# Kernel optimization log

Hardware: AMD Instinct MI355X
Metric: run time of the kernel (lower is better)

## Reference

```python
import jax, jax.numpy as jnp
import numpy as np

B, T, C, H, E, K = 4, 2048, 512, 2048, 8, 2


def setup_inputs() -> dict:
    key = jax.random.key(0)
    ks = jax.random.split(key, 7)
    s_r = 1.0 / np.sqrt(C)
    s_h = 1.0 / np.sqrt(H)
    return {
        "x": jax.random.normal(ks[0], (B, T, C), dtype=jnp.float32),
        "Wr": jax.random.uniform(ks[1], (C, E), jnp.float32, -s_r, s_r),
        "br": jax.random.uniform(ks[2], (E,), jnp.float32, -s_r, s_r),
        "W1": jax.random.uniform(ks[3], (E, C, H), jnp.float32, -s_r, s_r),
        "b1": jax.random.uniform(ks[4], (E, H), jnp.float32, -s_r, s_r),
        "W2": jax.random.uniform(ks[5], (E, H, C), jnp.float32, -s_h, s_h),
        "b2": jax.random.uniform(ks[6], (E, C), jnp.float32, -s_h, s_h),
    }


def reference(x, Wr, br, W1, b1, W2, b2):
    # Router logits [B,T,E]
    logits = jnp.einsum("btc,ce->bte", x, Wr) + br
    topk_vals, topk_idx = jax.lax.top_k(logits, K)  # [B,T,K]
    scores = jax.nn.softmax(topk_vals, axis=-1)  # softmax over the K selected
    # Combine weights per expert: gate[b,t,e] = sum_k scores[b,t,k]*(idx==e)
    onehot = jax.nn.one_hot(topk_idx, E, dtype=x.dtype)  # [B,T,K,E]
    gate = jnp.einsum("btk,btke->bte", scores, onehot)  # [B,T,E]
    # Dense-masked expert MLPs (tokens not routed to e have gate==0)
    h = jax.nn.relu(jnp.einsum("btc,ech->bteh", x, W1) + b1)  # [B,T,E,H]
    y = jnp.einsum("bteh,ehc->btec", h, W2) + b2  # [B,T,E,C]
    out = jnp.einsum("btec,bte->btc", y, gate)  # weighted combine
    return logits, topk_idx, out
```

## Files before the change

kernel.cpp:

```cpp
#include <hip/hip_runtime.h>
#include <hip/hip_bf16.h>

#define NTOK 8192
#define NASN 16384
#define C_ 512
#define H_ 2048
#define E_ 8
#define NCH 128
#define CHTOK 64
#define MAXT 136

typedef __bf16 bf16x8 __attribute__((ext_vector_type(8)));
typedef float f32x4 __attribute__((ext_vector_type(4)));

#define WS_COUNTS 0
#define WS_BASE   4096
#define WS_OFFS   8192
#define WS_T1S    8448
#define WS_INFO   8704
#define WS_TOKL   (WS_INFO + NTOK*16)
#define WS_SLOTS  (WS_TOKL + NASN*4)
#define WS_XBF    (WS_SLOTS + NTOK*8)
#define WS_W1B    (WS_XBF + (size_t)NTOK*C_*2)
#define WS_W2B    (WS_W1B + (size_t)E_*H_*C_*2)
#define WS_HS     (WS_W2B + (size_t)E_*H_*C_*2)
#define WS_YS     WS_XBF

__device__ __forceinline__ unsigned int f2bf(float f) {
  __hip_bfloat16 h = __float2bfloat16(f);
  return (unsigned int)*(unsigned short*)&h;
}
__device__ __forceinline__ float bf2f(unsigned int u) {
  return __int_as_float((u & 0xffffu) << 16);
}

__device__ __forceinline__ void g2l16(const unsigned short* g, unsigned short* l) {
  __builtin_amdgcn_global_load_lds(
      (const __attribute__((address_space(1))) unsigned int*)g,
      (__attribute__((address_space(3))) unsigned int*)l, 16, 0, 0);
}

__global__ __launch_bounds__(256) void k_router(
    const float* __restrict__ x, const float* __restrict__ Wr,
    const float* __restrict__ br, float* __restrict__ out_logits,
    float* __restrict__ out_idx, int4* __restrict__ info,
    int* __restrict__ counts, unsigned short* __restrict__ Xbf)
{
  int t = blockIdx.x * 4 + (threadIdx.x >> 6);
  int lane = threadIdx.x & 63;
  const float4* xr = (const float4*)(x + (size_t)t * C_);
  float4 x0 = xr[lane*2], x1 = xr[lane*2+1];
  uint4 pk;
  pk.x = f2bf(x0.x) | (f2bf(x0.y) << 16);
  pk.y = f2bf(x0.z) | (f2bf(x0.w) << 16);
  pk.z = f2bf(x1.x) | (f2bf(x1.y) << 16);
  pk.w = f2bf(x1.z) | (f2bf(x1.w) << 16);
  *(uint4*)(Xbf + (size_t)t * C_ + lane*8) = pk;

  float xs[8] = {x0.x,x0.y,x0.z,x0.w,x1.x,x1.y,x1.z,x1.w};
  float acc[8] = {0,0,0,0,0,0,0,0};
  #pragma unroll
  for (int j = 0; j < 8; j++) {
    const float4* w = (const float4*)(Wr + (size_t)(lane*8+j) * E_);
    float4 w0 = w[0], w1 = w[1];
    float we[8] = {w0.x,w0.y,w0.z,w0.w,w1.x,w1.y,w1.z,w1.w};
    #pragma unroll
    for (int e = 0; e < 8; e++) acc[e] += xs[j] * we[e];
  }
  #pragma unroll
  for (int off = 1; off < 64; off <<= 1) {
    #pragma unroll
    for (int e = 0; e < 8; e++) acc[e] += __shfl_xor(acc[e], off, 64);
  }
  #pragma unroll
  for (int e = 0; e < 8; e++) acc[e] += br[e];
  if (lane == 0) {
    #pragma unroll
    for (int e = 0; e < 8; e++) out_logits[t*8 + e] = acc[e];
    int i0 = 0; float v0 = acc[0];
    #pragma unroll
    for (int e = 1; e < 8; e++) if (acc[e] > v0) { v0 = acc[e]; i0 = e; }
    int i1 = -1; float v1 = -1e30f;
    #pragma unroll
    for (int e = 0; e < 8; e++) if (e != i0 && acc[e] > v1) { v1 = acc[e]; i1 = e; }
    float d = expf(v1 - v0);
    float s1 = d / (1.0f + d);
    float s0 = 1.0f - s1;
    out_idx[t*2]     = (float)i0;
    out_idx[t*2 + 1] = (float)i1;
    info[t] = make_int4(i0, i1, __float_as_int(s0), __float_as_int(s1));
    int ch = t >> 6;
    atomicAdd(&counts[ch*8 + i0], 1);
    atomicAdd(&counts[ch*8 + i1], 1);
  }
}

__global__ __launch_bounds__(256) void k_prefix(
    const int* __restrict__ counts, int* __restrict__ base,
    int* __restrict__ offs, int* __restrict__ t1s)
{
  __shared__ int lc[NCH*8];
  __shared__ int tot[8];
  __shared__ int off_s[9];
  int tid = threadIdx.x;
  for (int i = tid; i < NCH*8; i += 256) lc[i] = counts[i];
  __syncthreads();
  if (tid < 8) {
    int run = 0;
    for (int c = 0; c < NCH; c++) { int v = lc[c*8+tid]; lc[c*8+tid] = run; run += v; }
    tot[tid] = run;
  }
  __syncthreads();
  if (tid == 0) {
    int o = 0, t = 0;
    off_s[0] = 0; offs[0] = 0; t1s[0] = 0;
    for (int e = 0; e < 8; e++) {
      o += tot[e];
      off_s[e+1] = o; offs[e+1] = o;
      t += (tot[e] + 127) >> 7;
      t1s[e+1] = t;
    }
  }
  __syncthreads();
  for (int i = tid; i < NCH*8; i += 256) base[i] = off_s[i & 7] + lc[i];
}

__global__ __launch_bounds__(64) void k_scatter(
    const int4* __restrict__ info, const int* __restrict__ base,
    int* __restrict__ tokl, int2* __restrict__ slots2)
{
  __shared__ int cur[8];
  int c = blockIdx.x, tid = threadIdx.x;
  if (tid < 8) cur[tid] = base[c*8 + tid];
  __syncthreads();
  int t = c * CHTOK + tid;
  int4 nfo = info[t];
  int r0 = atomicAdd(&cur[nfo.x], 1);
  int r1 = atomicAdd(&cur[nfo.y], 1);
  tokl[r0] = t;
  tokl[r1] = t;
  slots2[t] = make_int2(r0, r1);
}

__global__ __launch_bounds__(256) void k_transpose(
    const float* __restrict__ in, unsigned short* __restrict__ outp, int R, int S)
{
  __shared__ float tile[32][33];
  size_t zo = (size_t)blockIdx.z * R * S;
  in += zo; outp += zo;
  int s0 = blockIdx.x * 32, r0 = blockIdx.y * 32;
  int tx = threadIdx.x, ty = threadIdx.y;
  #pragma unroll
  for (int i = 0; i < 4; i++)
    tile[ty + i*8][tx] = in[(size_t)(r0 + ty + i*8) * S + s0 + tx];
  __syncthreads();
  #pragma unroll
  for (int i = 0; i < 4; i++)
    outp[(size_t)(s0 + ty + i*8) * R + r0 + tx] = f2bf(tile[tx][ty + i*8]);
}

__global__ __launch_bounds__(256) void k_gemm1(
    const unsigned short* __restrict__ Xbf, const int* __restrict__ tokl,
    const unsigned short* __restrict__ W1b,
    const float* __restrict__ b1, unsigned short* __restrict__ Hs,
    const int* __restrict__ offs, const int* __restrict__ t1s)
{
  __shared__ __align__(16) unsigned short AB[2*128*64];
  unsigned short* Al = AB;
  unsigned short* Bl = AB + 128*64;
  int b = blockIdx.x;
  int mo = b >> 7, rr = b & 127;
  int n0 = (rr >> 3) * 128;
  int mt = mo*8 + (rr & 7);
  if (mt >= t1s[8]) return;
  int e = 0;
  #pragma unroll
  for (int i = 0; i < 7; i++) if (mt >= t1s[e+1]) e++;
  int row0 = offs[e] + (mt - t1s[e]) * 128;
  int rowEnd = offs[e+1];
  int tid = threadIdx.x, lane = tid & 63, w = tid >> 6;
  int wm = (w & 1) * 64, wn = (w >> 1) * 64;
  int quad = lane >> 4, l16 = lane & 15;
  const f32x4 zero = {0.f, 0.f, 0.f, 0.f};
  f32x4 acc[4][4];
  #pragma unroll
  for (int i = 0; i < 4; i++)
    #pragma unroll
    for (int j = 0; j < 4; j++) acc[i][j] = zero;
  const unsigned short* Bsrc = W1b + ((size_t)e * H_ + n0) * C_;

  const unsigned short* ga[4]; const unsigned short* gb[4];
  unsigned short* la[4]; unsigned short* lb[4];
  #pragma unroll
  for (int j = 0; j < 4; j++) {
    int L = (w*4 + j)*64 + lane;
    int row = L >> 3;
    int cc = (L & 7) ^ (row & 7);
    int gr = row0 + row; gr = gr < NASN-1 ? gr : NASN-1;
    int trow = tokl[gr];
    ga[j] = Xbf + (size_t)trow * C_ + cc*8;
    gb[j] = Bsrc + (size_t)row * C_ + cc*8;
    la[j] = Al + (w*4 + j)*512;
    lb[j] = Bl + (w*4 + j)*512;
  }
  int r7 = l16 & 7;

  for (int kk = 0; kk < C_; kk += 64) {
    #pragma unroll
    for (int j = 0; j < 4; j++) {
      g2l16(ga[j] + kk, la[j]);
      g2l16(gb[j] + kk, lb[j]);
    }
    __syncthreads();
    #pragma unroll
    for (int ks4 = 0; ks4 < 8; ks4 += 4) {
      int chunk = (ks4 + quad) ^ r7;
      bf16x8 af[4], bfr[4];
      #pragma unroll
      for (int i = 0; i < 4; i++)
        af[i] = *(const bf16x8*)&Al[(wm + i*16 + l16)*64 + chunk*8];
      #pragma unroll
      for (int j = 0; j < 4; j++)
        bfr[j] = *(const bf16x8*)&Bl[(wn + j*16 + l16)*64 + chunk*8];
      #pragma unroll
      for (int i = 0; i < 4; i++)
        #pragma unroll
        for (int j = 0; j < 4; j++)
          acc[i][j] = __builtin_amdgcn_mfma_f32_16x16x32_bf16(af[i], bfr[j], acc[i][j], 0, 0, 0);
    }
    __syncthreads();
  }

  unsigned short* Lt = AB + w*4096;
  #pragma unroll
  for (int j = 0; j < 4; j++) {
    int n = n0 + wn + j*16 + l16;
    float bias = b1[e * H_ + n];
    #pragma unroll
    for (int i = 0; i < 4; i++)
      #pragma unroll
      for (int r = 0; r < 4; r++) {
        float v = acc[i][j][r] + bias;
        Lt[(i*16 + quad*4 + r)*64 + j*16 + l16] = (unsigned short)f2bf(v > 0.f ? v : 0.f);
      }
  }
  #pragma unroll
  for (int it = 0; it < 8; it++) {
    int rloc = it*8 + (lane >> 3);
    int m = row0 + wm + rloc;
    uint4 vv = *(uint4*)&Lt[rloc*64 + (lane & 7)*8];
    if (m < rowEnd)
      *(uint4*)(Hs + (size_t)m * H_ + n0 + wn + (lane & 7)*8) = vv;
  }
}

__global__ __launch_bounds__(512) void k_gemm2(
    const unsigned short* __restrict__ Hs, const unsigned short* __restrict__ W2b,
    const float* __restrict__ b2, unsigned short* __restrict__ Ys,
    const int* __restrict__ offs, const int* __restrict__ t1s)
{
  __shared__ __align__(16) unsigned short AB[2*2*128*64];
  int b = blockIdx.x;
  int g = b >> 5, rr = b & 31;
  int n0 = (rr >> 3) * 128;
  int mt = g*8 + (rr & 7);
  if (mt >= t1s[8]) return;
  int e = 0;
  #pragma unroll
  for (int i = 0; i < 7; i++) if (mt >= t1s[e+1]) e++;
  int row0 = offs[e] + (mt - t1s[e]) * 128;
  int rowEnd = offs[e+1];
  int tid = threadIdx.x, lane = tid & 63, w = tid >> 6;
  int wq = w >> 1, kh = w & 1;
  int wm = (wq & 1) * 64, wn = (wq >> 1) * 64;
  int quad = lane >> 4, l16 = lane & 15;
  const f32x4 zero = {0.f, 0.f, 0.f, 0.f};
  f32x4 acc[4][4];
  #pragma unroll
  for (int i = 0; i < 4; i++)
    #pragma unroll
    for (int j = 0; j < 4; j++) acc[i][j] = zero;
  const unsigned short* Bsrc = W2b + ((size_t)e * C_ + n0) * H_;

  const unsigned short* ga[4]; const unsigned short* gb[4];
  unsigned short* la[4]; unsigned short* lb[4];
  #pragma unroll
  for (int j = 0; j < 4; j++) {
    int L = (wq*4 + j)*64 + lane;
    int row = L >> 3;
    int cc = (L & 7) ^ (row & 7);
    int gr = row0 + row; gr = gr < NASN-1 ? gr : NASN-1;
    ga[j] = Hs + (size_t)gr * H_ + kh*1024 + cc*8;
    gb[j] = Bsrc + (size_t)row * H_ + kh*1024 + cc*8;
    la[j] = AB + kh*16384 + (wq*4 + j)*512;
    lb[j] = AB + kh*16384 + 8192 + (wq*4 + j)*512;
  }
  int r7 = l16 & 7;
  const unsigned short* Ap = AB + kh*16384;
  const unsigned short* Bp = AB + kh*16384 + 8192;

  for (int kk = 0; kk < 1024; kk += 64) {
    #pragma unroll
    for (int j = 0; j < 4; j++) {
      g2l16(ga[j] + kk, la[j]);
      g2l16(gb[j] + kk, lb[j]);
    }
    __syncthreads();
    #pragma unroll
    for (int ks4 = 0; ks4 < 8; ks4 += 4) {
      int chunk = (ks4 + quad) ^ r7;
      bf16x8 af[4], bfr[4];
      #pragma unroll
      for (int i = 0; i < 4; i++)
        af[i] = *(const bf16x8*)&Ap[(wm + i*16 + l16)*64 + chunk*8];
      #pragma unroll
      for (int j = 0; j < 4; j++)
        bfr[j] = *(const bf16x8*)&Bp[(wn + j*16 + l16)*64 + chunk*8];
      #pragma unroll
      for (int i = 0; i < 4; i++)
        #pragma unroll
        for (int j = 0; j < 4; j++)
          acc[i][j] = __builtin_amdgcn_mfma_f32_16x16x32_bf16(af[i], bfr[j], acc[i][j], 0, 0, 0);
    }
    __syncthreads();
  }

  float* X = (float*)AB;
  if (kh == 1) {
    #pragma unroll
    for (int i = 0; i < 4; i++)
      #pragma unroll
      for (int j = 0; j < 4; j++) {
        int c = j*16 + l16;
        int slot = (i*4 + quad) ^ (c & 15);
        *(f32x4*)&X[wq*4096 + c*64 + slot*4] = acc[i][j];
      }
  }
  __syncthreads();
  if (kh == 0) {
    #pragma unroll
    for (int j = 0; j < 4; j++) {
      int c = j*16 + l16;
      float bias = b2[e * C_ + n0 + wn + c];
      #pragma unroll
      for (int i = 0; i < 4; i++) {
        int slot = (i*4 + quad) ^ (c & 15);
        f32x4 p = *(const f32x4*)&X[wq*4096 + c*64 + slot*4];
        #pragma unroll
        for (int r = 0; r < 4; r++) acc[i][j][r] += p[r] + bias;
      }
    }
  }
  __syncthreads();
  if (kh == 0) {
    unsigned short* Lt = AB + wq*4096;
    #pragma unroll
    for (int j = 0; j < 4; j++)
      #pragma unroll
      for (int i = 0; i < 4; i++)
        #pragma unroll
        for (int r = 0; r < 4; r++)
          Lt[(i*16 + quad*4 + r)*64 + j*16 + l16] =
              (unsigned short)f2bf(acc[i][j][r]);
    #pragma unroll
    for (int it = 0; it < 8; it++) {
      int rloc = it*8 + (lane >> 3);
      int m = row0 + wm + rloc;
      uint4 vv = *(uint4*)&Lt[rloc*64 + (lane & 7)*8];
      if (m < rowEnd)
        *(uint4*)(Ys + (size_t)m * C_ + n0 + wn + (lane & 7)*8) = vv;
    }
  }
}

__global__ __launch_bounds__(256) void k_combine(
    const unsigned short* __restrict__ Ys, const int4* __restrict__ info,
    const int2* __restrict__ slots2, float* __restrict__ outp)
{
  int t = blockIdx.x * 4 + (threadIdx.x >> 6);
  int lane = threadIdx.x & 63;
  int4 nfo = info[t];
  int2 ss = slots2[t];
  float g0 = __int_as_float(nfo.z), g1 = __int_as_float(nfo.w);
  uint4 a = *(const uint4*)(Ys + (size_t)ss.x * C_ + lane*8);
  uint4 bb = *(const uint4*)(Ys + (size_t)ss.y * C_ + lane*8);
  unsigned int au[4] = {a.x, a.y, a.z, a.w};
  unsigned int bu[4] = {bb.x, bb.y, bb.z, bb.w};
  float4 o0, o1;
  float* op = &o0.x;
  #pragma unroll
  for (int q = 0; q < 4; q++) {
    op[q*2 - (q>=2?0:0)] = 0;
  }
  float vals[8];
  #pragma unroll
  for (int q = 0; q < 4; q++) {
    vals[q*2]   = g0*bf2f(au[q])        + g1*bf2f(bu[q]);
    vals[q*2+1] = g0*bf2f(au[q] >> 16)  + g1*bf2f(bu[q] >> 16);
  }
  o0.x = vals[0]; o0.y = vals[1]; o0.z = vals[2]; o0.w = vals[3];
  o1.x = vals[4]; o1.y = vals[5]; o1.z = vals[6]; o1.w = vals[7];
  float4* o = (float4*)(outp + (size_t)t * C_ + lane*8);
  o[0] = o0;
  o[1] = o1;
}

extern "C" void kernel_launch(void* const* d_in, const int* in_sizes, int n_in,
                              void* d_out, int out_size, void* d_ws, size_t ws_size,
                              hipStream_t stream)
{
  const float* x  = (const float*)d_in[0];
  const float* Wr = (const float*)d_in[1];
  const float* br = (const float*)d_in[2];
  const float* W1 = (const float*)d_in[3];
  const float* b1 = (const float*)d_in[4];
  const float* W2 = (const float*)d_in[5];
  const float* b2 = (const float*)d_in[6];
  float* out = (float*)d_out;
  char* ws = (char*)d_ws;

  int*  counts = (int*)(ws + WS_COUNTS);
  int*  base   = (int*)(ws + WS_BASE);
  int*  offs   = (int*)(ws + WS_OFFS);
  int*  t1s    = (int*)(ws + WS_T1S);
  int4* info   = (int4*)(ws + WS_INFO);
  int*  tokl   = (int*)(ws + WS_TOKL);
  int2* slots2 = (int2*)(ws + WS_SLOTS);
  unsigned short* Xbf = (unsigned short*)(ws + WS_XBF);
  unsigned short* W1b = (unsigned short*)(ws + WS_W1B);
  unsigned short* W2b = (unsigned short*)(ws + WS_W2B);
  unsigned short* Hs  = (unsigned short*)(ws + WS_HS);
  unsigned short* Ys  = (unsigned short*)(ws + WS_YS);

  hipMemsetAsync(counts, 0, NCH*8*sizeof(int), stream);

  k_transpose<<<dim3(H_/32, C_/32, E_), dim3(32, 8), 0, stream>>>(W1, W1b, C_, H_);
  k_transpose<<<dim3(C_/32, H_/32, E_), dim3(32, 8), 0, stream>>>(W2, W2b, H_, C_);
  k_router<<<NTOK/4, 256, 0, stream>>>(x, Wr, br, out, out + 65536, info, counts, Xbf);
  k_prefix<<<1, 256, 0, stream>>>(counts, base, offs, t1s);
  k_scatter<<<NCH, 64, 0, stream>>>(info, base, tokl, slots2);
  k_gemm1<<<17*128, 256, 0, stream>>>(Xbf, tokl, W1b, b1, Hs, offs, t1s);
  k_gemm2<<<17*32, 512, 0, stream>>>(Hs, W2b, b2, Ys, offs, t1s);
  k_combine<<<NTOK/4, 256, 0, stream>>>(Ys, info, slots2, out + 81920);
}
```

Before: 305.7 us.

## Double-buffer GEMM K-loops and widen transpose tiles with vectorized bf16 stores

Both expert GEMMs now use a 32-wide K slice with two LDS buffers. The next slice's global-to-LDS copies are issued before computing the current one, and explicit vmcnt waits and barriers replace the two __syncthreads per step, so loads overlap with MFMA work. gemm2 drops its split-K across 512 threads and the cross-wave reduction through LDS, running 256 threads over the full H per block. That reduces waves per block and may lower latency hiding. The weight transpose now handles 128x32 tiles per block and writes four bf16 values per store.

```diff
diff --git a/kernel.cpp b/kernel.cpp
--- a/kernel.cpp
+++ b/kernel.cpp
@@ -8,7 +8,6 @@
 #define E_ 8
 #define NCH 128
 #define CHTOK 64
-#define MAXT 136
 
 typedef __bf16 bf16x8 __attribute__((ext_vector_type(8)));
 typedef float f32x4 __attribute__((ext_vector_type(4)));
@@ -145,18 +144,29 @@
 __global__ __launch_bounds__(256) void k_transpose(
     const float* __restrict__ in, unsigned short* __restrict__ outp, int R, int S)
 {
-  __shared__ float tile[32][33];
+  __shared__ float tile[128][33];
   size_t zo = (size_t)blockIdx.z * R * S;
   in += zo; outp += zo;
-  int s0 = blockIdx.x * 32, r0 = blockIdx.y * 32;
-  int tx = threadIdx.x, ty = threadIdx.y;
-  #pragma unroll
-  for (int i = 0; i < 4; i++)
-    tile[ty + i*8][tx] = in[(size_t)(r0 + ty + i*8) * S + s0 + tx];
+  int r0 = blockIdx.y * 128, s0 = blockIdx.x * 32;
+  int t = threadIdx.x;
+  #pragma unroll
+  for (int i = 0; i < 16; i++) {
+    int lin = i*256 + t;
+    int rr = lin >> 5, ss = lin & 31;
+    tile[rr][ss] = in[(size_t)(r0 + rr) * S + s0 + ss];
+  }
   __syncthreads();
   #pragma unroll
-  for (int i = 0; i < 4; i++)
-    outp[(size_t)(s0 + ty + i*8) * R + r0 + tx] = f2bf(tile[tx][ty + i*8]);
+  for (int i = 0; i < 4; i++) {
+    int lin = i*256 + t;
+    int ss = lin >> 5, rq = lin & 31;
+    ushort4 v;
+    v.x = (unsigned short)f2bf(tile[rq*4+0][ss]);
+    v.y = (unsigned short)f2bf(tile[rq*4+1][ss]);
+    v.z = (unsigned short)f2bf(tile[rq*4+2][ss]);
+    v.w = (unsigned short)f2bf(tile[rq*4+3][ss]);
+    *(ushort4*)(outp + (size_t)(s0 + ss) * R + r0 + rq*4) = v;
+  }
 }
 
 __global__ __launch_bounds__(256) void k_gemm1(
@@ -165,9 +175,7 @@
     const float* __restrict__ b1, unsigned short* __restrict__ Hs,
     const int* __restrict__ offs, const int* __restrict__ t1s)
 {
-  __shared__ __align__(16) unsigned short AB[2*128*64];
-  unsigned short* Al = AB;
-  unsigned short* Bl = AB + 128*64;
+  __shared__ __align__(16) unsigned short AB[2*8192];
   int b = blockIdx.x;
   int mo = b >> 7, rr = b & 127;
   int n0 = (rr >> 3) * 128;
@@ -189,46 +197,60 @@
     for (int j = 0; j < 4; j++) acc[i][j] = zero;
   const unsigned short* Bsrc = W1b + ((size_t)e * H_ + n0) * C_;
 
-  const unsigned short* ga[4]; const unsigned short* gb[4];
-  unsigned short* la[4]; unsigned short* lb[4];
-  #pragma unroll
-  for (int j = 0; j < 4; j++) {
-    int L = (w*4 + j)*64 + lane;
-    int row = L >> 3;
-    int cc = (L & 7) ^ (row & 7);
+  const unsigned short* ga[2]; const unsigned short* gb[2];
+  int lao[2], lbo[2];
+  #pragma unroll
+  for (int j = 0; j < 2; j++) {
+    int L = (w*2 + j)*64 + lane;
+    int row = L >> 2;
+    int gc = (L & 3) ^ (row & 3);
     int gr = row0 + row; gr = gr < NASN-1 ? gr : NASN-1;
     int trow = tokl[gr];
-    ga[j] = Xbf + (size_t)trow * C_ + cc*8;
-    gb[j] = Bsrc + (size_t)row * C_ + cc*8;
-    la[j] = Al + (w*4 + j)*512;
-    lb[j] = Bl + (w*4 + j)*512;
-  }
-  int r7 = l16 & 7;
-
-  for (int kk = 0; kk < C_; kk += 64) {
-    #pragma unroll
-    for (int j = 0; j < 4; j++) {
-      g2l16(ga[j] + kk, la[j]);
-      g2l16(gb[j] + kk, lb[j]);
+    ga[j] = Xbf + (size_t)trow * C_ + gc*8;
+    gb[j] = Bsrc + (size_t)row * C_ + gc*8;
+    lao[j] = (w*2 + j)*512;
+    lbo[j] = 4096 + (w*2 + j)*512;
+  }
+  int r3 = l16 & 3;
+  const int KI = C_ / 32;
+
+  #pragma unroll
+  for (int j = 0; j < 2; j++) { g2l16(ga[j], AB + lao[j]); g2l16(gb[j], AB + lbo[j]); }
+
+  for (int ki = 0; ki < KI; ki++) {
+    int p = ki & 1;
+    if (ki + 1 < KI) {
+      int off = (ki + 1) * 32;
+      unsigned short* nb = AB + (p ^ 1) * 8192;
+      #pragma unroll
+      for (int j = 0; j < 2; j++) {
+        g2l16(ga[j] + off, nb + lao[j]);
+        g2l16(gb[j] + off, nb + lbo[j]);
+      }
+      asm volatile("s_waitcnt vmcnt(4)" ::: "memory");
+    } else {
+      asm volatile("s_waitcnt vmcnt(0)" ::: "memory");
     }
-    __syncthreads();
-    #pragma unroll
-    for (int ks4 = 0; ks4 < 8; ks4 += 4) {
-      int chunk = (ks4 + quad) ^ r7;
-      bf16x8 af[4], bfr[4];
-      #pragma unroll
-      for (int i = 0; i < 4; i++)
-        af[i] = *(const bf16x8*)&Al[(wm + i*16 + l16)*64 + chunk*8];
+    asm volatile("s_barrier" ::: "memory");
+
+    const unsigned short* Ap = AB + p*8192;
+    const unsigned short* Bp = Ap + 4096;
+    int sl = (quad ^ r3) * 8;
+    bf16x8 af[4], bfr[4];
+    #pragma unroll
+    for (int i = 0; i < 4; i++)
+      af[i] = *(const bf16x8*)&Ap[(wm + i*16 + l16)*32 + sl];
+    #pragma unroll
+    for (int j = 0; j < 4; j++)
+      bfr[j] = *(const bf16x8*)&Bp[(wn + j*16 + l16)*32 + sl];
+    #pragma unroll
+    for (int i = 0; i < 4; i++)
       #pragma unroll
       for (int j = 0; j < 4; j++)
-        bfr[j] = *(const bf16x8*)&Bl[(wn + j*16 + l16)*64 + chunk*8];
-      #pragma unroll
-      for (int i = 0; i < 4; i++)
-        #pragma unroll
-        for (int j = 0; j < 4; j++)
-          acc[i][j] = __builtin_amdgcn_mfma_f32_16x16x32_bf16(af[i], bfr[j], acc[i][j], 0, 0, 0);
-    }
-    __syncthreads();
+        acc[i][j] = __builtin_amdgcn_mfma_f32_16x16x32_bf16(af[i], bfr[j], acc[i][j], 0, 0, 0);
+
+    asm volatile("s_waitcnt lgkmcnt(0)" ::: "memory");
+    asm volatile("s_barrier" ::: "memory");
   }
 
   unsigned short* Lt = AB + w*4096;
@@ -254,12 +276,12 @@
   }
 }
 
-__global__ __launch_bounds__(512) void k_gemm2(
+__global__ __launch_bounds__(256) void k_gemm2(
     const unsigned short* __restrict__ Hs, const unsigned short* __restrict__ W2b,
     const float* __restrict__ b2, unsigned short* __restrict__ Ys,
     const int* __restrict__ offs, const int* __restrict__ t1s)
 {
-  __shared__ __align__(16) unsigned short AB[2*2*128*64];
+  __shared__ __align__(16) unsigned short AB[2*8192];
   int b = blockIdx.x;
   int g = b >> 5, rr = b & 31;
   int n0 = (rr >> 3) * 128;
@@ -271,8 +293,7 @@
   int row0 = offs[e] + (mt - t1s[e]) * 128;
   int rowEnd = offs[e+1];
   int tid = threadIdx.x, lane = tid & 63, w = tid >> 6;
-  int wq = w >> 1, kh = w & 1;
-  int wm = (wq & 1) * 64, wn = (wq >> 1) * 64;
+  int wm = (w & 1) * 64, wn = (w >> 1) * 64;
   int quad = lane >> 4, l16 = lane & 15;
   const f32x4 zero = {0.f, 0.f, 0.f, 0.f};
   f32x4 acc[4][4];
@@ -282,94 +303,80 @@
     for (int j = 0; j < 4; j++) acc[i][j] = zero;
   const unsigned short* Bsrc = W2b + ((size_t)e * C_ + n0) * H_;
 
-  const unsigned short* ga[4]; const unsigned short* gb[4];
-  unsigned short* la[4]; unsigned short* lb[4];
+  const unsigned short* ga[2]; const unsigned short* gb[2];
+  int lao[2], lbo[2];
+  #pragma unroll
+  for (int j = 0; j < 2; j++) {
+    int L = (w*2 + j)*64 + lane;
+    int row = L >> 2;
+    int gc = (L & 3) ^ (row & 3);
+    int gr = row0 + row; gr = gr < NASN-1 ? gr : NASN-1;
+    ga[j] = Hs + (size_t)gr * H_ + gc*8;
+    gb[j] = Bsrc + (size_t)row * H_ + gc*8;
+    lao[j] = (w*2 + j)*512;
+    lbo[j] = 4096 + (w*2 + j)*512;
+  }
+  int r3 = l16 & 3;
+  const int KI = H_ / 32;
+
+  #pragma unroll
+  for (int j = 0; j < 2; j++) { g2l16(ga[j], AB + lao[j]); g2l16(gb[j], AB + lbo[j]); }
+
+  for (int ki = 0; ki < KI; ki++) {
+    int p = ki & 1;
+    if (ki + 1 < KI) {
+      int off = (ki + 1) * 32;
+      unsigned short* nb = AB + (p ^ 1) * 8192;
+      #pragma unroll
+      for (int j = 0; j < 2; j++) {
+        g2l16(ga[j] + off, nb + lao[j]);
+        g2l16(gb[j] + off, nb + lbo[j]);
+      }
+      asm volatile("s_waitcnt vmcnt(4)" ::: "memory");
+    } else {
+      asm volatile("s_waitcnt vmcnt(0)" ::: "memory");
+    }
+    asm volatile("s_barrier" ::: "memory");
+
+    const unsigned short* Ap = AB + p*8192;
+    const unsigned short* Bp = Ap + 4096;
+    int sl = (quad ^ r3) * 8;
+    bf16x8 af[4], bfr[4];
+    #pragma unroll
+    for (int i = 0; i < 4; i++)
+      af[i] = *(const bf16x8*)&Ap[(wm + i*16 + l16)*32 + sl];
+    #pragma unroll
+    for (int j = 0; j < 4; j++)
+      bfr[j] = *(const bf16x8*)&Bp[(wn + j*16 + l16)*32 + sl];
+    #pragma unroll
+    for (int i = 0; i < 4; i++)
+      #pragma unroll
+      for (int j = 0; j < 4; j++)
+        acc[i][j] = __builtin_amdgcn_mfma_f32_16x16x32_bf16(af[i], bfr[j], acc[i][j], 0, 0, 0);
+
+    asm volatile("s_waitcnt lgkmcnt(0)" ::: "memory");
+    asm volatile("s_barrier" ::: "memory");
+  }
+
+  unsigned short* Lt = AB + w*4096;
   #pragma unroll
   for (int j = 0; j < 4; j++) {
-    int L = (wq*4 + j)*64 + lane;
-    int row = L >> 3;
-    int cc = (L & 7) ^ (row & 7);
-    int gr = row0 + row; gr = gr < NASN-1 ? gr : NASN-1;
-    ga[j] = Hs + (size_t)gr * H_ + kh*1024 + cc*8;
-    gb[j] = Bsrc + (size_t)row * H_ + kh*1024 + cc*8;
-    la[j] = AB + kh*16384 + (wq*4 + j)*512;
-    lb[j] = AB + kh*16384 + 8192 + (wq*4 + j)*512;
-  }
-  int r7 = l16 & 7;
-  const unsigned short* Ap = AB + kh*16384;
-  const unsigned short* Bp = AB + kh*16384 + 8192;
-
-  for (int kk = 0; kk < 1024; kk += 64) {
-    #pragma unroll
-    for (int j = 0; j < 4; j++) {
-      g2l16(ga[j] + kk, la[j]);
-      g2l16(gb[j] + kk, lb[j]);
-    }
-    __syncthreads();
-    #pragma unroll
-    for (int ks4 = 0; ks4 < 8; ks4 += 4) {
-      int chunk = (ks4 + quad) ^ r7;
-      bf16x8 af[4], bfr[4];
-      #pragma unroll
-      for (int i = 0; i < 4; i++)
-        af[i] = *(const bf16x8*)&Ap[(wm + i*16 + l16)*64 + chunk*8];
-      #pragma unroll
-      for (int j = 0; j < 4; j++)
-        bfr[j] = *(const bf16x8*)&Bp[(wn + j*16 + l16)*64 + chunk*8];
-      #pragma unroll
-      for (int i = 0; i < 4; i++)
-        #pragma unroll
-        for (int j = 0; j < 4; j++)
-          acc[i][j] = __builtin_amdgcn_mfma_f32_16x16x32_bf16(af[i], bfr[j], acc[i][j], 0, 0, 0);
-    }
-    __syncthreads();
-  }
-
-  float* X = (float*)AB;
-  if (kh == 1) {
-    #pragma unroll
-    for (int i = 0; i < 4; i++)
-      #pragma unroll
-      for (int j = 0; j < 4; j++) {
-        int c = j*16 + l16;
-        int slot = (i*4 + quad) ^ (c & 15);
-        *(f32x4*)&X[wq*4096 + c*64 + slot*4] = acc[i][j];
-      }
-  }
-  __syncthreads();
-  if (kh == 0) {
-    #pragma unroll
-    for (int j = 0; j < 4; j++) {
-      int c = j*16 + l16;
-      float bias = b2[e * C_ + n0 + wn + c];
-      #pragma unroll
-      for (int i = 0; i < 4; i++) {
-        int slot = (i*4 + quad) ^ (c & 15);
-        f32x4 p = *(const f32x4*)&X[wq*4096 + c*64 + slot*4];
-        #pragma unroll
-        for (int r = 0; r < 4; r++) acc[i][j][r] += p[r] + bias;
-      }
-    }
-  }
-  __syncthreads();
-  if (kh == 0) {
-    unsigned short* Lt = AB + wq*4096;
-    #pragma unroll
-    for (int j = 0; j < 4; j++)
-      #pragma unroll
-      for (int i = 0; i < 4; i++)
-        #pragma unroll
-        for (int r = 0; r < 4; r++)
-          Lt[(i*16 + quad*4 + r)*64 + j*16 + l16] =
-              (unsigned short)f2bf(acc[i][j][r]);
-    #pragma unroll
-    for (int it = 0; it < 8; it++) {
-      int rloc = it*8 + (lane >> 3);
-      int m = row0 + wm + rloc;
-      uint4 vv = *(uint4*)&Lt[rloc*64 + (lane & 7)*8];
-      if (m < rowEnd)
-        *(uint4*)(Ys + (size_t)m * C_ + n0 + wn + (lane & 7)*8) = vv;
-    }
+    int n = n0 + wn + j*16 + l16;
+    float bias = b2[e * C_ + n];
+    #pragma unroll
+    for (int i = 0; i < 4; i++)
+      #pragma unroll
+      for (int r = 0; r < 4; r++)
+        Lt[(i*16 + quad*4 + r)*64 + j*16 + l16] =
+            (unsigned short)f2bf(acc[i][j][r] + bias);
+  }
+  #pragma unroll
+  for (int it = 0; it < 8; it++) {
+    int rloc = it*8 + (lane >> 3);
+    int m = row0 + wm + rloc;
+    uint4 vv = *(uint4*)&Lt[rloc*64 + (lane & 7)*8];
+    if (m < rowEnd)
+      *(uint4*)(Ys + (size_t)m * C_ + n0 + wn + (lane & 7)*8) = vv;
   }
 }
 
@@ -386,18 +393,13 @@
   uint4 bb = *(const uint4*)(Ys + (size_t)ss.y * C_ + lane*8);
   unsigned int au[4] = {a.x, a.y, a.z, a.w};
   unsigned int bu[4] = {bb.x, bb.y, bb.z, bb.w};
+  float vals[8];
+  #pragma unroll
+  for (int q = 0; q < 4; q++) {
+    vals[q*2]   = g0*bf2f(au[q])       + g1*bf2f(bu[q]);
+    vals[q*2+1] = g0*bf2f(au[q] >> 16) + g1*bf2f(bu[q] >> 16);
+  }
   float4 o0, o1;
-  float* op = &o0.x;
-  #pragma unroll
-  for (int q = 0; q < 4; q++) {
-    op[q*2 - (q>=2?0:0)] = 0;
-  }
-  float vals[8];
-  #pragma unroll
-  for (int q = 0; q < 4; q++) {
-    vals[q*2]   = g0*bf2f(au[q])        + g1*bf2f(bu[q]);
-    vals[q*2+1] = g0*bf2f(au[q] >> 16)  + g1*bf2f(bu[q] >> 16);
-  }
   o0.x = vals[0]; o0.y = vals[1]; o0.z = vals[2]; o0.w = vals[3];
   o1.x = vals[4]; o1.y = vals[5]; o1.z = vals[6]; o1.w = vals[7];
   float4* o = (float4*)(outp + (size_t)t * C_ + lane*8);
@@ -434,12 +436,12 @@
 
   hipMemsetAsync(counts, 0, NCH*8*sizeof(int), stream);
 
-  k_transpose<<<dim3(H_/32, C_/32, E_), dim3(32, 8), 0, stream>>>(W1, W1b, C_, H_);
-  k_transpose<<<dim3(C_/32, H_/32, E_), dim3(32, 8), 0, stream>>>(W2, W2b, H_, C_);
+  k_transpose<<<dim3(H_/32, C_/128, E_), 256, 0, stream>>>(W1, W1b, C_, H_);
+  k_transpose<<<dim3(C_/32, H_/128, E_), 256, 0, stream>>>(W2, W2b, H_, C_);
   k_router<<<NTOK/4, 256, 0, stream>>>(x, Wr, br, out, out + 65536, info, counts, Xbf);
   k_prefix<<<1, 256, 0, stream>>>(counts, base, offs, t1s);
   k_scatter<<<NCH, 64, 0, stream>>>(info, base, tokl, slots2);
   k_gemm1<<<17*128, 256, 0, stream>>>(Xbf, tokl, W1b, b1, Hs, offs, t1s);
-  k_gemm2<<<17*32, 512, 0, stream>>>(Hs, W2b, b2, Ys, offs, t1s);
+  k_gemm2<<<17*32, 256, 0, stream>>>(Hs, W2b, b2, Ys, offs, t1s);
   k_combine<<<NTOK/4, 256, 0, stream>>>(Ys, info, slots2, out + 81920);
 }
```

After: 279.6 us. -8.5%, faster.
